# Kernel optimization log

Measured on AMD Instinct MI355X. Metric: run time of the kernel, lower is better.

## Reference

```python
import jax, jax.numpy as jnp
from jax import lax
import numpy as np

B = 8192   # samples
L = 32     # predicted chars per sample (num_chars[i])
M = 32     # target labels per sample (num_labels[i])
C = 96     # character classes


def _edit_trace(pred, tgt):
    """Levenshtein DP + backtrace for one sample.
    pred: [L] int, tgt: [M] int.
    Returns (ti, tj, valid) of length L+M: 1-based (i,j) positions of the
    diagonal (match/substitute) moves on the optimal edit path, as emitted by
    distance_and_trace; valid masks non-diagonal / out-of-path steps."""
    Ls, Ms = pred.shape[0], tgt.shape[0]
    cost = (pred[:, None] != tgt[None, :]).astype(jnp.int32)  # [L,M]
    row0 = jnp.arange(Ms + 1, dtype=jnp.int32)

    def row_step(prev, crow):
        first = prev[0] + 1
        def col_step(left, z):
            up, diag, c = z
            v = jnp.minimum(jnp.minimum(up + 1, left + 1), diag + c)
            return v, v
        _, rest = lax.scan(col_step, first, (prev[1:], prev[:-1], crow))
        new = jnp.concatenate([first[None], rest])
        return new, new

    _, rows = lax.scan(row_step, row0, cost)
    D = jnp.concatenate([row0[None, :], rows], axis=0)  # [L+1, M+1]

    def bt_step(carry, _):
        i, j = carry
        c = cost[jnp.maximum(i - 1, 0), jnp.maximum(j - 1, 0)]
        dij = D[i, j]
        diag = (i > 0) & (j > 0) & (D[i - 1, j - 1] + c == dij)
        up = (~diag) & (i > 0) & (D[i - 1, j] + 1 == dij)
        left = (~diag) & (~up) & (j > 0)
        ni = i - (diag | up).astype(jnp.int32)
        nj = j - (diag | left).astype(jnp.int32)
        return (ni, nj), (i, j, diag)

    (_, _), (ti, tj, valid) = lax.scan(
        bt_step, (jnp.int32(Ls), jnp.int32(Ms)), None, length=Ls + Ms)
    return ti, tj, valid


def _forward(x, y, num_chars, num_labels):
    b = num_chars.shape[0]
    c = x.shape[1]
    l = x.shape[0] // b
    m = y.shape[0] // b
    logits = x.reshape(b, l, c)          # [B,L,C]
    labels = y.reshape(b, m)             # [B,M]
    pred = jnp.argmax(logits, axis=-1)   # torch.max(x,1) indices
    ti, tj, valid = jax.vmap(_edit_trace)(pred, labels)  # [B, L+M] each
    logp = jax.nn.log_softmax(logits, axis=-1)
    xi = jnp.where(valid, ti - 1, 0)     # trace[:,0]-1 (+ per-sample offset via reshape)
    yi = jnp.where(valid, tj - 1, 0)     # trace[:,1]-1
    lab = jnp.take_along_axis(labels, yi, axis=1)                 # [B,L+M]
    lp = jnp.take_along_axis(logp, xi[..., None], axis=1)         # [B,L+M,C]
    ce = -jnp.take_along_axis(lp, lab[..., None], axis=2)[..., 0]  # [B,L+M]
    cnt = valid.sum(axis=1)
    per_sample = jnp.where(valid, ce, 0.0).sum(axis=1) / jnp.maximum(cnt, 1)
    nonempty = cnt > 0                   # attenuation: skip empty traces
    total = jnp.where(nonempty, per_sample, 0.0).sum()
    return total / nonempty.sum()


def setup_inputs() -> dict:
    key = jax.random.key(0)
    k1, k2 = jax.random.split(key)
    x = jax.random.normal(k1, (B * L, C), dtype=jnp.float32)
    y = jax.random.randint(k2, (B * M,), 0, C, dtype=jnp.int32)
    num_chars = jnp.full((B,), L, dtype=jnp.int32)
    num_labels = jnp.full((B,), M, dtype=jnp.int32)
    return {"x": x, "y": y, "num_chars": num_chars, "num_labels": num_labels}


def reference(x, y, num_chars, num_labels):
    return _forward(x, y, num_chars, num_labels)
```

## Files before the change

### kernel.cpp

```cpp
#include <hip/hip_runtime.h>
#include <hip/hip_bf16.h>
#include <stdint.h>

#define BNUM  8192
#define LROWS 32
#define MLAB  32
#define CCLS  96
#define WPB   4

__global__ __launch_bounds__(256) void editloss_main(
    const float* __restrict__ x, const int* __restrict__ y,
    float* __restrict__ partial_sum, float* __restrict__ partial_cnt)
{
    __shared__ uint8_t        DS[WPB][33 * 33];
    __shared__ uint8_t        predS[WPB][LROWS];
    __shared__ uint8_t        labS[WPB][MLAB];
    __shared__ float          lseS[WPB][LROWS];
    __shared__ unsigned short traceS[WPB][LROWS + MLAB];
    __shared__ float          wsumS[WPB];
    __shared__ float          wcntS[WPB];

    const int w    = threadIdx.x >> 6;
    const int lane = threadIdx.x & 63;
    const int b    = blockIdx.x * WPB + w;

    const float* xs = x + (size_t)b * (LROWS * CCLS);

    if (lane < MLAB) labS[w][lane] = (uint8_t)y[b * MLAB + lane];

    const int g = lane >> 5;
    const int u = lane & 31;
    for (int pr = 0; pr < LROWS / 2; ++pr) {
        const int r = pr * 2 + g;
        const float* row = xs + r * CCLS;
        const float v0 = row[u * 3 + 0];
        const float v1 = row[u * 3 + 1];
        const float v2 = row[u * 3 + 2];
        float m = fmaxf(fmaxf(v0, v1), v2);
#pragma unroll
        for (int s = 16; s >= 1; s >>= 1) m = fmaxf(m, __shfl_xor(m, s));
        int cand = (v0 == m) ? (u * 3)
                 : (v1 == m) ? (u * 3 + 1)
                 : (v2 == m) ? (u * 3 + 2) : 4096;
#pragma unroll
        for (int s = 16; s >= 1; s >>= 1) cand = min(cand, __shfl_xor(cand, s));
        float se = __expf(v0 - m) + __expf(v1 - m) + __expf(v2 - m);
#pragma unroll
        for (int s = 16; s >= 1; s >>= 1) se += __shfl_xor(se, s);
        if (u == 0) {
            predS[w][r] = (uint8_t)cand;
            lseS[w][r]  = m + __logf(se);
        }
    }
    __syncthreads();

    const int j      = lane;
    const int labj   = (j >= 1 && j <= MLAB) ? (int)labS[w][j - 1] : 255;
    const int predrg = (lane < LROWS) ? (int)predS[w][lane] : 255;
    int prev = 0, prev2 = 0;
    if (lane == 0) DS[w][0] = 0;
    for (int d = 1; d <= LROWS + MLAB; ++d) {
        const int left  = __shfl_up(prev, 1);
        const int diagv = __shfl_up(prev2, 1);
        const int i = d - j;
        const int pi = __shfl(predrg, (i - 1) & 63);
        const int c = (pi != labj) ? 1 : 0;
        int cur = 0;
        if (j <= MLAB && i >= 0 && i <= LROWS) {
            if (i == 0)       cur = j;
            else if (j == 0)  cur = i;
            else              cur = min(min(prev, left) + 1, diagv + c);
            DS[w][i * 33 + j] = (uint8_t)cur;
        }
        prev2 = prev;
        prev  = cur;
    }
    __syncthreads();

    if (lane == 0) {
        int i = LROWS, jj = MLAB;
        for (int s = 0; s < LROWS + MLAB; ++s) {
            const int dij = DS[w][i * 33 + jj];
            bool dg = false;
            if (i > 0 && jj > 0) {
                const int c = (predS[w][i - 1] != labS[w][jj - 1]) ? 1 : 0;
                dg = ((int)DS[w][(i - 1) * 33 + (jj - 1)] + c == dij);
            }
            bool up = false;
            if (!dg && i > 0) up = ((int)DS[w][(i - 1) * 33 + jj] + 1 == dij);
            const bool lf = !dg && !up && (jj > 0);
            traceS[w][s] = (unsigned short)((i << 7) | (jj << 1) | (dg ? 1 : 0));
            if (dg || up) --i;
            if (dg || lf) --jj;
        }
    }
    __syncthreads();

    const unsigned t = traceS[w][lane];
    float ce = 0.f;
    int cnt = 0;
    if (t & 1u) {
        const int jj = (t >> 1) & 63;
        const int i  = (int)(t >> 7);
        const int labv = labS[w][jj - 1];
        const float xv = xs[(i - 1) * CCLS + labv];
        ce = lseS[w][i - 1] - xv;
        cnt = 1;
    }
#pragma unroll
    for (int s = 32; s >= 1; s >>= 1) {
        ce  += __shfl_xor(ce, s);
        cnt += __shfl_xor(cnt, s);
    }
    if (lane == 0) {
        wsumS[w] = (cnt > 0) ? (ce / (float)cnt) : 0.f;
        wcntS[w] = (cnt > 0) ? 1.f : 0.f;
    }
    __syncthreads();
    if (threadIdx.x == 0) {
        float s = 0.f, c2 = 0.f;
        for (int k = 0; k < WPB; ++k) { s += wsumS[k]; c2 += wcntS[k]; }
        partial_sum[blockIdx.x] = s;
        partial_cnt[blockIdx.x] = c2;
    }
}

__global__ __launch_bounds__(256) void editloss_finalize(
    const float* __restrict__ partial_sum, const float* __restrict__ partial_cnt,
    float* __restrict__ out, int nblocks)
{
    float s = 0.f, c = 0.f;
    for (int k = threadIdx.x; k < nblocks; k += 256) {
        s += partial_sum[k];
        c += partial_cnt[k];
    }
#pragma unroll
    for (int d = 32; d >= 1; d >>= 1) {
        s += __shfl_xor(s, d);
        c += __shfl_xor(c, d);
    }
    __shared__ float ss[4], cc[4];
    const int w = threadIdx.x >> 6, lane = threadIdx.x & 63;
    if (lane == 0) { ss[w] = s; cc[w] = c; }
    __syncthreads();
    if (threadIdx.x == 0) {
        const float S  = ss[0] + ss[1] + ss[2] + ss[3];
        const float C2 = cc[0] + cc[1] + cc[2] + cc[3];
        out[0] = (C2 > 0.f) ? (S / C2) : 0.f;
    }
}

extern "C" void kernel_launch(void* const* d_in, const int* in_sizes, int n_in,
                              void* d_out, int out_size, void* d_ws, size_t ws_size,
                              hipStream_t stream) {
    const float* x = (const float*)d_in[0];
    const int*   y = (const int*)d_in[1];
    float* out = (float*)d_out;

    float* partial_sum = (float*)d_ws;
    float* partial_cnt = partial_sum + 2048;

    const int nblocks = BNUM / WPB;
    editloss_main<<<nblocks, 256, 0, stream>>>(x, y, partial_sum, partial_cnt);
    editloss_finalize<<<1, 256, 0, stream>>>(partial_sum, partial_cnt, out, nblocks);
}
```

Measured before the change: 194.9 us.

## Fuse edit-distance backtrace into forward DP with path-carried CE sums

Replaces the stored DP table plus serial single-lane backtrace with a forward wavefront that carries, for each cell, the diagonal-match count and accumulated cross-entropy along the path the backtrace would choose. Each half-wave now processes one sample, and a per-sample table of CE values for every (row, label) pair is precomputed during the softmax pass, with the sign encoding the mismatch cost. This removes the long serial backtrace and the gather pass, but it computes CE for all 32x32 pairs and uses more shared memory per block. Tie-breaking in the forward pass has to reproduce the backtrace's diag>up>left priority from the end cell, which may not always match.

```diff
diff --git a/kernel.cpp b/kernel.cpp
--- a/kernel.cpp
+++ b/kernel.cpp
@@ -7,121 +7,100 @@
 #define MLAB  32
 #define CCLS  96
 #define WPB   4
+#define SPW   2
+#define SPB   (WPB*SPW)
+#define NBLK  (BNUM/SPB)
 
 __global__ __launch_bounds__(256) void editloss_main(
     const float* __restrict__ x, const int* __restrict__ y,
     float* __restrict__ partial_sum, float* __restrict__ partial_cnt)
 {
-    __shared__ uint8_t        DS[WPB][33 * 33];
-    __shared__ uint8_t        predS[WPB][LROWS];
-    __shared__ uint8_t        labS[WPB][MLAB];
-    __shared__ float          lseS[WPB][LROWS];
-    __shared__ unsigned short traceS[WPB][LROWS + MLAB];
-    __shared__ float          wsumS[WPB];
-    __shared__ float          wcntS[WPB];
+    __shared__ float ceTab[SPB][LROWS * MLAB];
+    __shared__ float psum[SPB];
+    __shared__ float pcnt[SPB];
 
     const int w    = threadIdx.x >> 6;
     const int lane = threadIdx.x & 63;
-    const int b    = blockIdx.x * WPB + w;
+    const int g    = lane >> 5;
+    const int u    = lane & 31;
+    const int s    = w * SPW + g;
+    const int sb   = blockIdx.x * SPB + s;
 
-    const float* xs = x + (size_t)b * (LROWS * CCLS);
+    const float* xs    = x + (size_t)sb * (LROWS * CCLS);
+    const int    lab_u = y[sb * MLAB + u];
 
-    if (lane < MLAB) labS[w][lane] = (uint8_t)y[b * MLAB + lane];
-
-    const int g = lane >> 5;
-    const int u = lane & 31;
-    for (int pr = 0; pr < LROWS / 2; ++pr) {
-        const int r = pr * 2 + g;
+    for (int r = 0; r < LROWS; ++r) {
         const float* row = xs + r * CCLS;
         const float v0 = row[u * 3 + 0];
         const float v1 = row[u * 3 + 1];
         const float v2 = row[u * 3 + 2];
+        const float xg = row[lab_u];
         float m = fmaxf(fmaxf(v0, v1), v2);
 #pragma unroll
-        for (int s = 16; s >= 1; s >>= 1) m = fmaxf(m, __shfl_xor(m, s));
+        for (int t = 16; t >= 1; t >>= 1) m = fmaxf(m, __shfl_xor(m, t));
         int cand = (v0 == m) ? (u * 3)
                  : (v1 == m) ? (u * 3 + 1)
                  : (v2 == m) ? (u * 3 + 2) : 4096;
 #pragma unroll
-        for (int s = 16; s >= 1; s >>= 1) cand = min(cand, __shfl_xor(cand, s));
+        for (int t = 16; t >= 1; t >>= 1) cand = min(cand, __shfl_xor(cand, t));
         float se = __expf(v0 - m) + __expf(v1 - m) + __expf(v2 - m);
 #pragma unroll
-        for (int s = 16; s >= 1; s >>= 1) se += __shfl_xor(se, s);
-        if (u == 0) {
-            predS[w][r] = (uint8_t)cand;
-            lseS[w][r]  = m + __logf(se);
-        }
+        for (int t = 16; t >= 1; t >>= 1) se += __shfl_xor(se, t);
+        const float lse = m + __logf(se);
+        const float ce  = lse - xg;
+        ceTab[s][r * MLAB + u] = (cand == lab_u) ? ce : -ce;
     }
     __syncthreads();
 
-    const int j      = lane;
-    const int labj   = (j >= 1 && j <= MLAB) ? (int)labS[w][j - 1] : 255;
-    const int predrg = (lane < LROWS) ? (int)predS[w][lane] : 255;
-    int prev = 0, prev2 = 0;
-    if (lane == 0) DS[w][0] = 0;
+    const int j = u + 1;
+    int   prevW = 0;   float prevCE = 0.f;
+    int   diagW = 0;   float diagCE = 0.f;
     for (int d = 1; d <= LROWS + MLAB; ++d) {
-        const int left  = __shfl_up(prev, 1);
-        const int diagv = __shfl_up(prev2, 1);
+        const int   lWs  = __shfl_up(prevW, 1);
+        const float lCEs = __shfl_up(prevCE, 1);
         const int i = d - j;
-        const int pi = __shfl(predrg, (i - 1) & 63);
-        const int c = (pi != labj) ? 1 : 0;
-        int cur = 0;
-        if (j <= MLAB && i >= 0 && i <= LROWS) {
-            if (i == 0)       cur = j;
-            else if (j == 0)  cur = i;
-            else              cur = min(min(prev, left) + 1, diagv + c);
-            DS[w][i * 33 + j] = (uint8_t)cur;
+        const int   lW  = (u == 0) ? max(i, 0)     : lWs;
+        const float lCE = (u == 0) ? 0.f           : lCEs;
+        const int   dW  = (u == 0) ? max(i - 1, 0) : diagW;
+        const float dCE = (u == 0) ? 0.f           : diagCE;
+        int curW; float curCE;
+        if (i <= 0) {
+            curW = j; curCE = 0.f;
+        } else if (i > LROWS) {
+            curW = prevW; curCE = prevCE;
+        } else {
+            const int uD = prevW & 255, uC = prevW >> 8;
+            const int lD = lW & 255,    lC = lW >> 8;
+            const int dD = dW & 255,    dC = dW >> 8;
+            const float ct  = ceTab[s][(i - 1) * MLAB + (j - 1)];
+            const int   c   = (ct < 0.f) ? 1 : 0;
+            const float cev = fabsf(ct);
+            const int nD = min(min(uD, lD) + 1, dD + c);
+            const bool dg = (dD + c == nD);
+            const bool up = !dg && (uD + 1 == nD);
+            int nC; float nCE;
+            if (dg)      { nC = dC + 1; nCE = dCE + cev; }
+            else if (up) { nC = uC;     nCE = prevCE;    }
+            else         { nC = lC;     nCE = lCE;       }
+            curW = nD | (nC << 8);
+            curCE = nCE;
         }
-        prev2 = prev;
-        prev  = cur;
+        diagW = lWs; diagCE = lCEs;
+        prevW = curW; prevCE = curCE;
     }
-    __syncthreads();
 
-    if (lane == 0) {
-        int i = LROWS, jj = MLAB;
-        for (int s = 0; s < LROWS + MLAB; ++s) {
-            const int dij = DS[w][i * 33 + jj];
-            bool dg = false;
-            if (i > 0 && jj > 0) {
-                const int c = (predS[w][i - 1] != labS[w][jj - 1]) ? 1 : 0;
-                dg = ((int)DS[w][(i - 1) * 33 + (jj - 1)] + c == dij);
-            }
-            bool up = false;
-            if (!dg && i > 0) up = ((int)DS[w][(i - 1) * 33 + jj] + 1 == dij);
-            const bool lf = !dg && !up && (jj > 0);
-            traceS[w][s] = (unsigned short)((i << 7) | (jj << 1) | (dg ? 1 : 0));
-            if (dg || up) --i;
-            if (dg || lf) --jj;
-        }
-    }
-    __syncthreads();
-
-    const unsigned t = traceS[w][lane];
-    float ce = 0.f;
-    int cnt = 0;
-    if (t & 1u) {
-        const int jj = (t >> 1) & 63;
-        const int i  = (int)(t >> 7);
-        const int labv = labS[w][jj - 1];
-        const float xv = xs[(i - 1) * CCLS + labv];
-        ce = lseS[w][i - 1] - xv;
-        cnt = 1;
-    }
-#pragma unroll
-    for (int s = 32; s >= 1; s >>= 1) {
-        ce  += __shfl_xor(ce, s);
-        cnt += __shfl_xor(cnt, s);
-    }
-    if (lane == 0) {
-        wsumS[w] = (cnt > 0) ? (ce / (float)cnt) : 0.f;
-        wcntS[w] = (cnt > 0) ? 1.f : 0.f;
+    if (u == 31) {
+        const int cnt = prevW >> 8;
+        psum[s] = (cnt > 0) ? prevCE / (float)cnt : 0.f;
+        pcnt[s] = (cnt > 0) ? 1.f : 0.f;
     }
     __syncthreads();
     if (threadIdx.x == 0) {
-        float s = 0.f, c2 = 0.f;
-        for (int k = 0; k < WPB; ++k) { s += wsumS[k]; c2 += wcntS[k]; }
-        partial_sum[blockIdx.x] = s;
-        partial_cnt[blockIdx.x] = c2;
+        float ss = 0.f, cc = 0.f;
+#pragma unroll
+        for (int k = 0; k < SPB; ++k) { ss += psum[k]; cc += pcnt[k]; }
+        partial_sum[blockIdx.x] = ss;
+        partial_cnt[blockIdx.x] = cc;
     }
 }
 
@@ -158,9 +137,8 @@
     float* out = (float*)d_out;
 
     float* partial_sum = (float*)d_ws;
-    float* partial_cnt = partial_sum + 2048;
+    float* partial_cnt = partial_sum + NBLK;
 
-    const int nblocks = BNUM / WPB;
-    editloss_main<<<nblocks, 256, 0, stream>>>(x, y, partial_sum, partial_cnt);
-    editloss_finalize<<<1, 256, 0, stream>>>(partial_sum, partial_cnt, out, nblocks);
+    editloss_main<<<NBLK, 256, 0, stream>>>(x, y, partial_sum, partial_cnt);
+    editloss_finalize<<<1, 256, 0, stream>>>(partial_sum, partial_cnt, out, NBLK);
 }
```

After: 176.3 us. -9.5%, faster.
